# Kernel tuning notes

Measured on AMD Instinct MI355X. Metric: run time of the kernel, lower is better.

## Reference

```python
import jax, jax.numpy as jnp
import numpy as np

B, V, T = 8, 25, 128
C, NH, DK = 256, 8, 32      # hidden_size = NH*DK; dv == dk (required by residual shapes)
DFF, IT = 1024, 4           # FFN hidden (d_in), num_layers
EPS_LN, EPS_BN, SLOPE = 1e-6, 1e-5, 0.01
SCALE = np.float32(1.0 / np.sqrt(DK))


def setup_inputs():
    ks = iter(jax.random.split(jax.random.key(0), 40))
    def w(shape, s=0.05):
        return jax.random.normal(next(ks), shape, jnp.float32) * s
    inp = {'data': jax.random.normal(next(ks), (B, C, V, T), jnp.float32)}
    inp['ln_g'] = jnp.ones((IT, C)); inp['ln_b'] = jnp.zeros((IT, C))
    for p in ('tj', 'tr'):
        for nm in ('q', 'k', 'v'):
            inp[p + '_w' + nm] = w((IT, C, C))
            inp[p + '_b' + nm] = jnp.zeros((IT, C))
        inp[p + '_bn_g'] = jnp.ones((IT, C)); inp[p + '_bn_b'] = jnp.zeros((IT, C))
        inp[p + '_w1'] = w((IT, DFF, C)); inp[p + '_b1'] = jnp.zeros((IT, DFF))
        inp[p + '_w2'] = w((IT, C, DFF)); inp[p + '_b2'] = jnp.zeros((IT, C))
        inp[p + '_fbn_g'] = jnp.ones((IT, C)); inp[p + '_fbn_b'] = jnp.zeros((IT, C))
    return inp


def _bn(x, g, b, axes):
    # train-mode BatchNorm: batch stats, biased variance; channel axis = 1
    m = x.mean(axes, keepdims=True)
    v = ((x - m) ** 2).mean(axes, keepdims=True)
    sh = [1] * x.ndim; sh[1] = -1
    return (x - m) * jax.lax.rsqrt(v + EPS_BN) * g.reshape(sh) + b.reshape(sh)


def _ffn(x, w1, b1, w2, b2, fg, fb):
    # PositionFeedForward on x: [N, C, L] -> [N, C, L]
    xt = jnp.swapaxes(x, 1, 2)                                   # [N, L, C]
    h = jax.nn.relu(jnp.einsum('nlc,fc->nlf', xt, w1) + b1)
    o = jnp.einsum('nlf,cf->nlc', h, w2) + b2 + xt               # residual
    return _bn(jnp.swapaxes(o, 1, 2), fg, fb, (0, 2))


def _tju(x, ax, wq, bq, wk, bk, wv, bv, bn_g, bn_b, w1, b1, w2, b2, fg, fb):
    # sliding-window (3) self-attn + 2 relay tokens; x: [N,C,T], ax: [N,C,2,T]
    N = x.shape[0]
    q = (jnp.einsum('oc,nct->not', wq, x) + bq[:, None]).reshape(N, NH, DK, T)
    k = (jnp.einsum('oc,nct->not', wk, x) + bk[:, None]).reshape(N, NH, DK, T)
    v = (jnp.einsum('oc,nct->not', wv, x) + bv[:, None]).reshape(N, NH, DK, T)
    kp = jnp.pad(k, ((0, 0), (0, 0), (0, 0), (1, 1)))
    vp = jnp.pad(v, ((0, 0), (0, 0), (0, 0), (1, 1)))
    kw = jnp.stack([kp[..., u:u + T] for u in range(3)], axis=3)  # [N,NH,DK,3,T]
    vw = jnp.stack([vp[..., u:u + T] for u in range(3)], axis=3)
    ak = (jnp.einsum('oc,ncat->noat', wk, ax) + bk[:, None, None]).reshape(N, NH, DK, 2, T)
    av = (jnp.einsum('oc,ncat->noat', wv, ax) + bv[:, None, None]).reshape(N, NH, DK, 2, T)
    kk = jnp.concatenate([kw, ak], axis=3)                        # [N,NH,DK,5,T]
    vv = jnp.concatenate([vw, av], axis=3)
    a = jax.nn.softmax(jnp.einsum('nhdt,nhdwt->nhwt', q, kk) * SCALE, axis=2)
    att = jnp.einsum('nhwt,nhdwt->nhdt', a, vv).reshape(N, C, T)
    ret = _bn(x + att, bn_g, bn_b, (0, 2))
    return _ffn(ret, w1, b1, w2, b2, fg, fb)


def _tru(r, y, wq, bq, wk, bk, wv, bv, bn_g, bn_b, w1, b1, w2, b2, fg, fb):
    # relay cross-attention; r: [N,C], y: [N,C,L]
    N, _, L = y.shape
    q = (r @ wq.T + bq).reshape(N, NH, DK)
    k = (jnp.einsum('oc,ncl->nol', wk, y) + bk[:, None]).reshape(N, NH, DK, L)
    v = (jnp.einsum('oc,ncl->nol', wv, y) + bv[:, None]).reshape(N, NH, DK, L)
    a = jax.nn.softmax(jnp.einsum('nhd,nhdl->nhl', q, k) * SCALE, axis=-1)
    att = jnp.einsum('nhl,nhdl->nhd', a, v).reshape(N, C)
    ret = _bn((r + att)[:, :, None], bn_g, bn_b, (0, 2))          # BN over batch
    return _ffn(ret, w1, b1, w2, b2, fg, fb)[:, :, 0]


def _forward(data, ln_g, ln_b, tj, tr):
    N = B * V
    embs = jnp.transpose(data, (0, 2, 1, 3)).reshape(N, C, T)
    nodes, relay = embs, embs.mean(2)                             # relay: [N,C]
    for i in range(IT):
        ax = jnp.concatenate([embs[:, :, None, :],
                              jnp.broadcast_to(relay[:, :, None, None], (N, C, 1, T))], axis=2)
        m = nodes.mean(1, keepdims=True)
        vv = nodes.var(1, keepdims=True)
        xln = (nodes - m) * jax.lax.rsqrt(vv + EPS_LN) * ln_g[i][None, :, None] + ln_b[i][None, :, None]
        nodes = jax.nn.leaky_relu(_tju(xln, ax, *[p[i] for p in tj]), SLOPE)
        y = jnp.concatenate([relay[:, :, None], nodes], axis=2)   # [N,C,T+1]
        relay = jax.nn.leaky_relu(_tru(relay, y, *[p[i] for p in tr]), SLOPE)
    return nodes.reshape(B, V, C, T)


def reference(data, ln_g, ln_b,
              tj_wq, tj_bq, tj_wk, tj_bk, tj_wv, tj_bv, tj_bn_g, tj_bn_b,
              tj_w1, tj_b1, tj_w2, tj_b2, tj_fbn_g, tj_fbn_b,
              tr_wq, tr_bq, tr_wk, tr_bk, tr_wv, tr_bv, tr_bn_g, tr_bn_b,
              tr_w1, tr_b1, tr_w2, tr_b2, tr_fbn_g, tr_fbn_b):
    tj = (tj_wq, tj_bq, tj_wk, tj_bk, tj_wv, tj_bv, tj_bn_g, tj_bn_b,
          tj_w1, tj_b1, tj_w2, tj_b2, tj_fbn_g, tj_fbn_b)
    tr = (tr_wq, tr_bq, tr_wk, tr_bk, tr_wv, tr_bv, tr_bn_g, tr_bn_b,
          tr_w1, tr_b1, tr_w2, tr_b2, tr_fbn_g, tr_fbn_b)
    return _forward(data, ln_g, ln_b, tj, tr)
```

## Files before the change

### kernel.cpp

```cpp
#include <hip/hip_runtime.h>
#include <cstddef>

#define BB   8
#define VV   25
#define TT   128
#define CC   256
#define NHH  8
#define DKK  32
#define DFFF 1024
#define ITER 4
#define NN   (BB*VV)
#define NT   (NN*TT)
#define LL1  (TT+1)
#define EPS_LN 1e-6f
#define EPS_BN 1e-5f
#define SLOPE  0.01f
#define SCALE_F 0.17677669529663687f

typedef unsigned short ushort_t;
typedef __attribute__((ext_vector_type(8))) short short8;
typedef __attribute__((ext_vector_type(4))) short short4_t;
typedef __attribute__((ext_vector_type(4))) float floatx4;

union U8 { short8 v; ushort_t u[8]; };

__device__ __forceinline__ float bf2f(ushort_t u) {
    union { unsigned int i; float f; } x; x.i = ((unsigned int)u) << 16; return x.f;
}
__device__ __forceinline__ ushort_t f2bf(float f) {
    union { float f; unsigned int i; } x; x.f = f;
    unsigned int r = x.i + 0x7FFFu + ((x.i >> 16) & 1u);
    return (ushort_t)(r >> 16);
}
__device__ __forceinline__ float2 bn_fin(float s, float ss) {
    float m = s * (1.0f/NT);
    float var = ss * (1.0f/NT) - m*m; if (var < 0.f) var = 0.f;
    return make_float2(m, rsqrtf(var + EPS_BN));
}

__device__ __forceinline__ void gl_lds16(const ushort_t* g, ushort_t* l) {
    __builtin_amdgcn_global_load_lds(
        (const __attribute__((address_space(1))) unsigned int*)g,
        (__attribute__((address_space(3))) unsigned int*)l,
        16, 0, 0);
}

__device__ __forceinline__ void ld32(const ushort_t* p, float* q) {
    #pragma unroll
    for (int c8 = 0; c8 < 4; c8++) {
        U8 u; u.v = *(const short8*)(p + c8*8);
        #pragma unroll
        for (int j = 0; j < 8; j++) q[c8*8+j] = bf2f(u.u[j]);
    }
}
__device__ __forceinline__ float dot32(const ushort_t* p, const float* q) {
    float s = 0.f;
    #pragma unroll
    for (int c8 = 0; c8 < 4; c8++) {
        U8 u; u.v = *(const short8*)(p + c8*8);
        #pragma unroll
        for (int j = 0; j < 8; j++) s += q[c8*8+j]*bf2f(u.u[j]);
    }
    return s;
}
__device__ __forceinline__ void acc32(const ushort_t* p, float e, float* av) {
    #pragma unroll
    for (int c8 = 0; c8 < 4; c8++) {
        U8 u; u.v = *(const short8*)(p + c8*8);
        #pragma unroll
        for (int j = 0; j < 8; j++) av[c8*8+j] += e*bf2f(u.u[j]);
    }
}

__global__ __launch_bounds__(256) void k_zero(float* __restrict__ p, int n)
{
    int i = blockIdx.x*256 + threadIdx.x;
    if (i < n) p[i] = 0.f;
}
__global__ __launch_bounds__(256) void k_cast2(const float* __restrict__ src,
    ushort_t* __restrict__ dst, int per, int dstride, int total)
{
    int i = blockIdx.x*256 + threadIdx.x;
    if (i < total) dst[(size_t)(i/per)*dstride + (i%per)] = f2bf(src[i]);
}
__global__ __launch_bounds__(256) void k_copy2(const float* __restrict__ src,
    float* __restrict__ dst, int per, int dstride, int total)
{
    int i = blockIdx.x*256 + threadIdx.x;
    if (i < total) dst[(size_t)(i/per)*dstride + (i%per)] = src[i];
}

__global__ __launch_bounds__(128) void k_embed(const float* __restrict__ data,
    float* __restrict__ nodesf, ushort_t* __restrict__ embs_bf, float* __restrict__ relay)
{
    __shared__ float tile[32][TT+1];
    int cc0 = blockIdx.x*32, n = blockIdx.y;
    int b = n / VV, v = n % VV, t = threadIdx.x;
    for (int cl = 0; cl < 32; cl++)
        tile[cl][t] = data[(((size_t)b*CC + cc0 + cl)*VV + v)*TT + t];
    __syncthreads();
    if (t < 32) {
        float s = 0.f;
        for (int tt = 0; tt < TT; tt++) s += tile[t][tt];
        relay[n*CC + cc0 + t] = s * (1.0f/TT);
    }
    #pragma unroll 8
    for (int it = 0; it < 32; it++) {
        int t_l = it*4 + (t >> 5), c_l = t & 31;
        float val = tile[c_l][t_l];
        size_t o = (size_t)(n*TT + t_l)*CC + cc0 + c_l;
        nodesf[o] = val;
        embs_bf[o] = f2bf(val);
    }
}

__global__ __launch_bounds__(256) void k_layernorm(float* __restrict__ x,
    ushort_t* __restrict__ outb, const float* __restrict__ g, const float* __restrict__ b)
{
    int wave = threadIdx.x >> 6, lane = threadIdx.x & 63;
    size_t base = (size_t)(blockIdx.x*4 + wave)*CC + lane*4;
    float4 v = *(float4*)&x[base];
    float s  = v.x + v.y + v.z + v.w;
    float ss = v.x*v.x + v.y*v.y + v.z*v.z + v.w*v.w;
    #pragma unroll
    for (int o = 32; o; o >>= 1) { s += __shfl_xor(s, o); ss += __shfl_xor(ss, o); }
    float m = s * (1.0f/CC);
    float var = ss * (1.0f/CC) - m*m; if (var < 0.f) var = 0.f;
    float rs = rsqrtf(var + EPS_LN);
    float4 gg = *(const float4*)&g[lane*4];
    float4 bb = *(const float4*)&b[lane*4];
    v.x = (v.x - m)*rs*gg.x + bb.x;
    v.y = (v.y - m)*rs*gg.y + bb.y;
    v.z = (v.z - m)*rs*gg.z + bb.z;
    v.w = (v.w - m)*rs*gg.w + bb.w;
    *(float4*)&x[base] = v;
    ushort_t o4[4] = {f2bf(v.x), f2bf(v.y), f2bf(v.z), f2bf(v.w)};
    *(short4_t*)&outb[base] = *(short4_t*)o4;
}

#define FL_RELU  1
#define FL_BF16  2
#define FL_RESBN 4
#define FL_HM    8

#define STAGE(SA, SB, T_) do {                                              \
    ushort_t* db_ = isA ? (SA) : (SB);                                      \
    gl_lds16(gSrc[0] + (T_)*32, &db_[dstOff[0]]);                           \
    gl_lds16(gSrc[1] + (T_)*32, &db_[dstOff[1]]);                           \
    } while (0)

#define COMPUTE(SA, SB) do {                                                \
    short8 af_[4], bf_[2];                                                  \
    _Pragma("unroll")                                                       \
    for (int mi_ = 0; mi_ < 4; mi_++)                                       \
        af_[mi_] = *(const short8*)&SA[aOff[mi_]];                          \
    _Pragma("unroll")                                                       \
    for (int ni_ = 0; ni_ < 2; ni_++)                                       \
        bf_[ni_] = *(const short8*)&SB[bOff[ni_]];                          \
    _Pragma("unroll")                                                       \
    for (int mi_ = 0; mi_ < 4; mi_++)                                       \
        _Pragma("unroll")                                                   \
        for (int ni_ = 0; ni_ < 2; ni_++)                                   \
            acc[mi_][ni_] = __builtin_amdgcn_mfma_f32_16x16x32_bf16(        \
                bf_[ni_], af_[mi_], acc[mi_][ni_], 0, 0, 0);                \
    } while (0)

#define WAITVL(S_) asm volatile("s_waitcnt vmcnt(" S_ ") lgkmcnt(0)" ::: "memory")

#define PHASE(CA, CB, PA, PB, T_) do {                                      \
    if ((T_) + 2 < NK) STAGE(PA, PB, (T_) + 2);                             \
    COMPUTE(CA, CB);                                                        \
    if ((T_) + 1 < NK) {                                                    \
        __builtin_amdgcn_sched_barrier(0);                                  \
        if ((T_) + 2 < NK) WAITVL("2");                                     \
        else               WAITVL("0");                                     \
        __builtin_amdgcn_s_barrier();                                       \
        __builtin_amdgcn_sched_barrier(0);                                  \
    }                                                                       \
    } while (0)

template<int K, int STATS>
__global__ __launch_bounds__(512) void k_gemm_mfma(
    const ushort_t* A, const ushort_t* B, const float* bias,
    const float* rx, const float* __restrict__ rawms,
    const float* __restrict__ bng, const float* __restrict__ bnb,
    float* outf, ushort_t* outb, int ostride, int ntiles_n, int flags,
    const ushort_t* A2, const ushort_t* B2, const float* bias2,
    ushort_t* outb2, int ostride2, int ntiles_n2,
    float* stats_acc)
{
    __shared__ ushort_t sA0[128*32];
    __shared__ ushort_t sB0[128*32];
    __shared__ ushort_t sA1[128*32];
    __shared__ ushort_t sB1[128*32];
    __shared__ ushort_t sA2[128*32];
    __shared__ ushort_t sB2[128*32];
    const int pid = blockIdx.x;
    const int xcd = pid & 7, idx = pid >> 3;
    const int ntile_tot = ntiles_n + ntiles_n2;
    const int nt_i = idx % ntile_tot;
    const int m0 = (xcd*25 + idx/ntile_tot) * 128;
    const ushort_t* Ap;  const ushort_t* Bp;  const float* biasp;
    ushort_t* outbp;  int ostridep, n0;
    if (nt_i < ntiles_n) {
        Ap = A;  Bp = B;  biasp = bias;  outbp = outb;
        ostridep = ostride;  n0 = nt_i*128;
    } else {
        Ap = A2; Bp = B2; biasp = bias2; outbp = outb2;
        ostridep = ostride2; n0 = (nt_i - ntiles_n)*128;
    }
    const int tid = threadIdx.x;
    const int lane = tid & 63, wave = tid >> 6;
    const int wm = (wave & 1) * 64, wn = (wave >> 1) * 32;
    const int fr = lane >> 4, fc = lane & 15;

    const bool isA = (wave < 4);
    const ushort_t* gSrc[2];
    int dstOff[2];
    #pragma unroll
    for (int j = 0; j < 2; j++) {
        int s  = wave*2 + j;
        int sl = isA ? s : s - 8;
        int c  = sl*64 + lane;
        int row = c >> 2;
        int kcs = ((c & 3) - (row >> 1)) & 3;
        gSrc[j] = (isA ? Ap + (size_t)(m0 + row)*K
                       : Bp + (size_t)(n0 + row)*K) + kcs*8;
        dstOff[j] = sl*512;
    }
    int aOff[4], bOff[2];
    #pragma unroll
    for (int mi = 0; mi < 4; mi++) {
        int row = wm + mi*16 + fc;
        aOff[mi] = row*32 + (((fr + (row >> 1)) & 3) * 8);
    }
    #pragma unroll
    for (int ni = 0; ni < 2; ni++) {
        int row = wn + ni*16 + fc;
        bOff[ni] = row*32 + (((fr + (row >> 1)) & 3) * 8);
    }

    floatx4 acc[4][2];
    #pragma unroll
    for (int i = 0; i < 4; i++)
        #pragma unroll
        for (int j = 0; j < 2; j++) acc[i][j] = (floatx4){0.f,0.f,0.f,0.f};

    constexpr int NK = K >> 5;
    STAGE(sA0, sB0, 0);
    if (NK > 1) STAGE(sA1, sB1, 1);
    __builtin_amdgcn_sched_barrier(0);
    if (NK > 1) WAITVL("2");
    else        WAITVL("0");
    __builtin_amdgcn_s_barrier();
    __builtin_amdgcn_sched_barrier(0);

    #pragma unroll
    for (int tb = 0; tb < NK; tb += 3) {
        PHASE(sA0, sB0, sA2, sB2, tb);
        if (tb + 1 < NK) PHASE(sA1, sB1, sA0, sB0, tb + 1);
        if (tb + 2 < NK) PHASE(sA2, sB2, sA1, sB1, tb + 2);
    }

    float st[2][4], sst[2][4];
    if constexpr (STATS) {
        #pragma unroll
        for (int a = 0; a < 2; a++)
            #pragma unroll
            for (int b2_ = 0; b2_ < 4; b2_++) { st[a][b2_] = 0.f; sst[a][b2_] = 0.f; }
    }
    #pragma unroll
    for (int ni = 0; ni < 2; ni++) {
        int nb = n0 + wn + ni*16 + fr*4;
        float4 bias4 = *(const float4*)&biasp[nb];
        float bm[4] = {0,0,0,0}, bs[4] = {0,0,0,0}, bb2[4] = {0,0,0,0};
        if (flags & FL_RESBN) {
            float4 s1 = *(const float4*)&rawms[nb];
            float4 s2 = *(const float4*)&rawms[CC + nb];
            float4 g4 = *(const float4*)&bng[nb];
            float4 b4 = *(const float4*)&bnb[nb];
            float2 f0 = bn_fin(s1.x, s2.x); float2 f1 = bn_fin(s1.y, s2.y);
            float2 f2 = bn_fin(s1.z, s2.z); float2 f3 = bn_fin(s1.w, s2.w);
            bm[0]=f0.x; bm[1]=f1.x; bm[2]=f2.x; bm[3]=f3.x;
            bs[0]=f0.y*g4.x; bs[1]=f1.y*g4.y; bs[2]=f2.y*g4.z; bs[3]=f3.y*g4.w;
            bb2[0]=b4.x; bb2[1]=b4.y; bb2[2]=b4.z; bb2[3]=b4.w;
        }
        float bia[4] = {bias4.x, bias4.y, bias4.z, bias4.w};
        size_t hm_base = ((size_t)(nb >> 5) * NT) * 32 + (nb & 31);
        #pragma unroll
        for (int mi = 0; mi < 4; mi++) {
            int m = m0 + wm + mi*16 + fc;
            size_t idx2 = (flags & FL_HM) ? hm_base + (size_t)m*32
                                          : (size_t)m*ostridep + nb;
            float vals[4];
            #pragma unroll
            for (int r = 0; r < 4; r++) vals[r] = acc[mi][ni][r] + bia[r];
            if (flags & FL_RESBN) {
                float4 rx4 = *(const float4*)&rx[idx2];
                float rxa[4] = {rx4.x, rx4.y, rx4.z, rx4.w};
                #pragma unroll
                for (int r = 0; r < 4; r++)
                    vals[r] += (rxa[r] - bm[r])*bs[r] + bb2[r];
            }
            if (flags & FL_RELU)
                #pragma unroll
                for (int r = 0; r < 4; r++) vals[r] = fmaxf(vals[r], 0.f);
            if constexpr (STATS) {
                #pragma unroll
                for (int r = 0; r < 4; r++) {
                    st[ni][r] += vals[r];
                    sst[ni][r] += vals[r]*vals[r];
                }
            }
            if (flags & FL_BF16) {
                ushort_t o4[4] = {f2bf(vals[0]), f2bf(vals[1]),
                                  f2bf(vals[2]), f2bf(vals[3])};
                *(short4_t*)&outbp[idx2] = *(short4_t*)o4;
            } else {
                float4 ov = make_float4(vals[0], vals[1], vals[2], vals[3]);
                *(float4*)&outf[idx2] = ov;
            }
        }
    }
    if constexpr (STATS) {
        #pragma unroll
        for (int ni = 0; ni < 2; ni++)
            #pragma unroll
            for (int r = 0; r < 4; r++) {
                float s_ = st[ni][r], ss_ = sst[ni][r];
                #pragma unroll
                for (int msk = 1; msk < 16; msk <<= 1) {
                    s_  += __shfl_xor(s_,  msk);
                    ss_ += __shfl_xor(ss_, msk);
                }
                st[ni][r] = s_; sst[ni][r] = ss_;
            }
        if (fc == 0) {
            #pragma unroll
            for (int ni = 0; ni < 2; ni++)
                #pragma unroll
                for (int r = 0; r < 4; r++) {
                    int ch = n0 + wn + ni*16 + fr*4 + r;
                    atomicAdd(&stats_acc[ch],      st[ni][r]);
                    atomicAdd(&stats_acc[CC + ch], sst[ni][r]);
                }
        }
    }
}

__global__ __launch_bounds__(256) void k_sgemm(
    const float* __restrict__ W, const float* __restrict__ X,
    const float* __restrict__ bias, const float* __restrict__ res,
    float* __restrict__ out, int K, int OUT, int do_relu)
{
    __shared__ float sW[16][260];
    __shared__ float sX[16][260];
    int o0 = blockIdx.x*16, n0 = blockIdx.y*16;
    int tx = threadIdx.x, ty = threadIdx.y;
    int tid = ty*16 + tx;
    float acc0 = 0.f, acc1 = 0.f;
    for (int kc = 0; kc < K; kc += 256) {
        #pragma unroll
        for (int j = 0; j < 4; j++) {
            int lin = tid + j*256;
            int row = lin >> 6, c4 = (lin & 63)*4;
            *(float4*)&sW[row][c4] = *(const float4*)&W[(size_t)(o0+row)*K + kc + c4];
            float4 xv = make_float4(0.f,0.f,0.f,0.f);
            if (n0 + row < NN) xv = *(const float4*)&X[(size_t)(n0+row)*K + kc + c4];
            *(float4*)&sX[row][c4] = xv;
        }
        __syncthreads();
        #pragma unroll 8
        for (int k4 = 0; k4 < 64; k4 += 2) {
            float4 w0 = *(const float4*)&sW[tx][k4*4];
            float4 x0 = *(const float4*)&sX[ty][k4*4];
            float4 w1 = *(const float4*)&sW[tx][k4*4+4];
            float4 x1 = *(const float4*)&sX[ty][k4*4+4];
            acc0 += w0.x*x0.x + w0.y*x0.y + w0.z*x0.z + w0.w*x0.w;
            acc1 += w1.x*x1.x + w1.y*x1.y + w1.z*x1.z + w1.w*x1.w;
        }
        __syncthreads();
    }
    float accv = acc0 + acc1;
    int o = o0 + tx, n = n0 + ty;
    if (n < NN) {
        float val = accv + bias[o];
        if (res) val += res[(size_t)n*OUT + o];
        if (do_relu) val = fmaxf(val, 0.f);
        out[(size_t)n*OUT + o] = val;
    }
}

__global__ __launch_bounds__(128) void k_attn_tj(
    const ushort_t* __restrict__ qkv, const ushort_t* __restrict__ ekv,
    const float* __restrict__ rel, const float* __restrict__ xln,
    float* __restrict__ out)
{
    int t = threadIdx.x, h = blockIdx.x, n = blockIdx.y;
    int nt = n*TT + t;
    const ushort_t* qp = qkv + ((size_t)h*NT       + nt)*32;
    const ushort_t* kp = qkv + ((size_t)(8+h)*NT   + nt)*32;
    const ushort_t* vp = qkv + ((size_t)(16+h)*NT  + nt)*32;
    const ushort_t* ep = ekv + ((size_t)h*NT       + nt)*32;
    const ushort_t* evp= ekv + ((size_t)(8+h)*NT   + nt)*32;
    const float*    rp = rel + n*1280 + h*32;

    float qv[32];
    ld32(qp, qv);
    float s0 = 0.f, s1, s2 = 0.f, s3, s4 = 0.f;
    s1 = dot32(kp, qv);
    s3 = dot32(ep, qv);
    #pragma unroll
    for (int j = 0; j < 8; j++) {
        float4 rv4 = *(const float4*)&rp[j*4];
        s4 += qv[j*4]*rv4.x + qv[j*4+1]*rv4.y + qv[j*4+2]*rv4.z + qv[j*4+3]*rv4.w;
    }
    if (t > 0)    s0 = dot32(kp - 32, qv);
    if (t < TT-1) s2 = dot32(kp + 32, qv);

    s0 *= SCALE_F; s1 *= SCALE_F; s2 *= SCALE_F; s3 *= SCALE_F; s4 *= SCALE_F;
    float mx = fmaxf(fmaxf(fmaxf(s0, s1), fmaxf(s2, s3)), s4);
    float e0 = expf(s0-mx), e1 = expf(s1-mx), e2 = expf(s2-mx), e3 = expf(s3-mx), e4 = expf(s4-mx);
    float inv = 1.f/(e0+e1+e2+e3+e4);
    e0 *= inv; e1 *= inv; e2 *= inv; e3 *= inv; e4 *= inv;

    float av[32];
    #pragma unroll
    for (int d = 0; d < 32; d++) av[d] = 0.f;
    acc32(vp, e1, av);
    acc32(evp, e3, av);
    if (t > 0)    acc32(vp - 32, e0, av);
    if (t < TT-1) acc32(vp + 32, e2, av);
    #pragma unroll
    for (int j = 0; j < 8; j++) {
        float4 rv4 = *(const float4*)&rp[256 + j*4];
        av[j*4] += e4*rv4.x; av[j*4+1] += e4*rv4.y; av[j*4+2] += e4*rv4.z; av[j*4+3] += e4*rv4.w;
    }
    const float* xp = xln + (size_t)nt*CC + h*32;
    float* op = out + (size_t)nt*CC + h*32;
    #pragma unroll
    for (int j = 0; j < 8; j++) {
        float4 xv = *(const float4*)&xp[j*4];
        float4 ov;
        ov.x = xv.x + av[j*4]; ov.y = xv.y + av[j*4+1];
        ov.z = xv.z + av[j*4+2]; ov.w = xv.w + av[j*4+3];
        *(float4*)&op[j*4] = ov;
    }
}

__global__ __launch_bounds__(256) void k_bnstats_tm(const float* __restrict__ x,
    float* __restrict__ accum)
{
    __shared__ float lds[8][256];
    int w = threadIdx.x >> 6, lane = threadIdx.x & 63;
    size_t base = (size_t)blockIdx.x*TT*CC;
    float s[4] = {0,0,0,0}, ss[4] = {0,0,0,0};
    for (int tok = w; tok < TT; tok += 4) {
        float4 v = *(const float4*)&x[base + (size_t)tok*CC + lane*4];
        s[0] += v.x; s[1] += v.y; s[2] += v.z; s[3] += v.w;
        ss[0] += v.x*v.x; ss[1] += v.y*v.y; ss[2] += v.z*v.z; ss[3] += v.w*v.w;
    }
    #pragma unroll
    for (int j = 0; j < 4; j++) { lds[w][lane*4+j] = s[j]; lds[4+w][lane*4+j] = ss[j]; }
    __syncthreads();
    int c = threadIdx.x;
    float ps  = lds[0][c]+lds[1][c]+lds[2][c]+lds[3][c];
    float pss = lds[4][c]+lds[5][c]+lds[6][c]+lds[7][c];
    atomicAdd(&accum[c], ps);
    atomicAdd(&accum[CC + c], pss);
}

__global__ __launch_bounds__(256) void k_bn_apply_raw(const float* __restrict__ x,
    const float* __restrict__ acc, const float* __restrict__ g, const float* __restrict__ b,
    ushort_t* __restrict__ outb)
{
    size_t base = ((size_t)blockIdx.x*256 + threadIdx.x)*4;
    int c0 = (int)(base & (CC-1));
    float4 v  = *(const float4*)&x[base];
    float4 a1 = *(const float4*)&acc[c0];
    float4 a2 = *(const float4*)&acc[CC + c0];
    float4 g4 = *(const float4*)&g[c0];
    float4 b4 = *(const float4*)&b[c0];
    float vals[4] = {v.x,v.y,v.z,v.w};
    float s1v[4] = {a1.x,a1.y,a1.z,a1.w};
    float s2v[4] = {a2.x,a2.y,a2.z,a2.w};
    float gg[4] = {g4.x,g4.y,g4.z,g4.w};
    float bb[4] = {b4.x,b4.y,b4.z,b4.w};
    ushort_t o4[4];
    #pragma unroll
    for (int j = 0; j < 4; j++) {
        float2 f = bn_fin(s1v[j], s2v[j]);
        o4[j] = f2bf((vals[j] - f.x)*f.y*gg[j] + bb[j]);
    }
    *(short4_t*)&outb[base] = *(short4_t*)o4;
}

__global__ __launch_bounds__(256) void k_bn_ln(const float* __restrict__ x,
    const float* __restrict__ acc, const float* __restrict__ fg, const float* __restrict__ fb,
    const float* __restrict__ lg, const float* __restrict__ lb,
    float* __restrict__ xlnf, ushort_t* __restrict__ xlnb, ushort_t* __restrict__ nodesb)
{
    int wave = threadIdx.x >> 6, lane = threadIdx.x & 63;
    int c0 = lane*4;
    size_t base = (size_t)(blockIdx.x*4 + wave)*CC + c0;
    float4 v  = *(const float4*)&x[base];
    float4 a1 = *(const float4*)&acc[c0];
    float4 a2 = *(const float4*)&acc[CC + c0];
    float4 g4 = *(const float4*)&fg[c0];
    float4 b4 = *(const float4*)&fb[c0];
    float vals[4] = {v.x,v.y,v.z,v.w};
    float s1v[4] = {a1.x,a1.y,a1.z,a1.w};
    float s2v[4] = {a2.x,a2.y,a2.z,a2.w};
    float gg[4] = {g4.x,g4.y,g4.z,g4.w};
    float bb[4] = {b4.x,b4.y,b4.z,b4.w};
    ushort_t nb4[4];
    #pragma unroll
    for (int j = 0; j < 4; j++) {
        float2 f = bn_fin(s1v[j], s2v[j]);
        float vv = (vals[j] - f.x)*f.y*gg[j] + bb[j];
        vv = vv > 0.f ? vv : SLOPE*vv;
        vals[j] = vv;
        nb4[j] = f2bf(vv);
    }
    *(short4_t*)&nodesb[base] = *(short4_t*)nb4;
    float s  = vals[0]+vals[1]+vals[2]+vals[3];
    float ss = vals[0]*vals[0]+vals[1]*vals[1]+vals[2]*vals[2]+vals[3]*vals[3];
    #pragma unroll
    for (int o = 32; o; o >>= 1) { s += __shfl_xor(s, o); ss += __shfl_xor(ss, o); }
    float m = s * (1.0f/CC);
    float var = ss * (1.0f/CC) - m*m; if (var < 0.f) var = 0.f;
    float rs = rsqrtf(var + EPS_LN);
    float4 lg4 = *(const float4*)&lg[c0];
    float4 lb4 = *(const float4*)&lb[c0];
    float lgv[4] = {lg4.x,lg4.y,lg4.z,lg4.w};
    float lbv[4] = {lb4.x,lb4.y,lb4.z,lb4.w};
    float4 xo;
    ushort_t xb4[4];
    float t0 = (vals[0]-m)*rs*lgv[0] + lbv[0];
    float t1 = (vals[1]-m)*rs*lgv[1] + lbv[1];
    float t2 = (vals[2]-m)*rs*lgv[2] + lbv[2];
    float t3 = (vals[3]-m)*rs*lgv[3] + lbv[3];
    xo.x = t0; xo.y = t1; xo.z = t2; xo.w = t3;
    xb4[0]=f2bf(t0); xb4[1]=f2bf(t1); xb4[2]=f2bf(t2); xb4[3]=f2bf(t3);
    *(float4*)&xlnf[base] = xo;
    *(short4_t*)&xlnb[base] = *(short4_t*)xb4;
}

__global__ __launch_bounds__(256) void k_bn_out_t(const float* __restrict__ x,
    const float* __restrict__ acc, const float* __restrict__ g, const float* __restrict__ b,
    float* __restrict__ out)
{
    __shared__ float tile[64][65];
    int nt0 = blockIdx.x*64, c0 = blockIdx.y*64;
    int w = threadIdx.x >> 6, lane = threadIdx.x & 63;
    int n = nt0 >> 7, t0 = nt0 & 127;
    int c = c0 + lane;
    float2 f = bn_fin(acc[c], acc[CC + c]);
    float gg = f.y*g[c], mm = f.x, bb = b[c];
    #pragma unroll
    for (int it = 0; it < 16; it++) {
        int tok = it*4 + w;
        float v = x[(size_t)(nt0 + tok)*CC + c];
        v = (v - mm)*gg + bb;
        v = v > 0.f ? v : SLOPE*v;
        tile[tok][lane] = v;
    }
    __syncthreads();
    #pragma unroll
    for (int it = 0; it < 16; it++) {
        int c_l = it*4 + w;
        out[(size_t)(n*CC + c0 + c_l)*TT + t0 + lane] = tile[lane][c_l];
    }
}

__global__ __launch_bounds__(64) void k_bn_relay(const float* __restrict__ x,
    float* __restrict__ out, const float* __restrict__ g, const float* __restrict__ b, int leaky)
{
    int c = blockIdx.x, tid = threadIdx.x;
    float s = 0.f, ss = 0.f;
    for (int n = tid; n < NN; n += 64) { float v = x[(size_t)n*CC + c]; s += v; ss += v*v; }
    for (int off = 32; off; off >>= 1) { s += __shfl_down(s, off); ss += __shfl_down(ss, off); }
    float S = __shfl(s, 0), SS = __shfl(ss, 0);
    float m = S / NN;
    float var = SS / NN - m*m; if (var < 0.f) var = 0.f;
    float rs = rsqrtf(var + EPS_BN);
    float gg = g[c]*rs, bb = b[c];
    for (int n = tid; n < NN; n += 64) {
        float v = (x[(size_t)n*CC + c] - m)*gg + bb;
        if (leaky) v = v > 0.f ? v : SLOPE*v;
        out[(size_t)n*CC + c] = v;
    }
}

__global__ __launch_bounds__(64) void k_attn_tr(
    const float* __restrict__ rel, const float* __restrict__ ykv,
    const float* __restrict__ relay, float* __restrict__ out)
{
    int h = blockIdx.x, n = blockIdx.y, tid = threadIdx.x;
    __shared__ float sc[LL1];
    __shared__ float red[64][33];
    float q0[32];
    const float* qp = rel + (size_t)n*1280 + 1024 + h*32;
    #pragma unroll
    for (int j = 0; j < 8; j++) {
        float4 v = *(const float4*)&qp[j*4];
        q0[j*4] = v.x; q0[j*4+1] = v.y; q0[j*4+2] = v.z; q0[j*4+3] = v.w;
    }
    for (int l = tid; l < LL1; l += 64) {
        const float* kp = (l == 0) ? (rel + (size_t)n*1280 + 512 + h*32)
                                   : (ykv + ((size_t)h*NT + n*TT + l-1)*32);
        float s = 0.f;
        #pragma unroll
        for (int j = 0; j < 8; j++) {
            float4 v = *(const float4*)&kp[j*4];
            s += q0[j*4]*v.x + q0[j*4+1]*v.y + q0[j*4+2]*v.z + q0[j*4+3]*v.w;
        }
        sc[l] = s * SCALE_F;
    }
    __syncthreads();
    float mx = -1e30f;
    for (int l = tid; l < LL1; l += 64) mx = fmaxf(mx, sc[l]);
    for (int off = 32; off; off >>= 1) mx = fmaxf(mx, __shfl_xor(mx, off));
    float sum = 0.f;
    for (int l = tid; l < LL1; l += 64) { float e = expf(sc[l]-mx); sc[l] = e; sum += e; }
    for (int off = 32; off; off >>= 1) sum += __shfl_xor(sum, off);
    __syncthreads();
    float av[32];
    #pragma unroll
    for (int d = 0; d < 32; d++) av[d] = 0.f;
    for (int l = tid; l < LL1; l += 64) {
        float e = sc[l];
        const float* vp = (l == 0) ? (rel + (size_t)n*1280 + 768 + h*32)
                                   : (ykv + ((size_t)(8+h)*NT + n*TT + l-1)*32);
        #pragma unroll
        for (int j = 0; j < 8; j++) {
            float4 v = *(const float4*)&vp[j*4];
            av[j*4] += e*v.x; av[j*4+1] += e*v.y; av[j*4+2] += e*v.z; av[j*4+3] += e*v.w;
        }
    }
    #pragma unroll
    for (int d = 0; d < 32; d++) red[tid][d] = av[d];
    __syncthreads();
    if (tid < 32) {
        float a = 0.f;
        for (int k = 0; k < 64; k++) a += red[k][tid];
        a /= sum;
        int idx = n*CC + h*32 + tid;
        out[idx] = relay[idx] + a;
    }
}

extern "C" void kernel_launch(void* const* d_in, const int* in_sizes, int n_in,
                              void* d_out, int out_size, void* d_ws, size_t ws_size,
                              hipStream_t stream)
{
    const float* data    = (const float*)d_in[0];
    const float* ln_g    = (const float*)d_in[1];
    const float* ln_b    = (const float*)d_in[2];
    const float* tj_wq   = (const float*)d_in[3];
    const float* tj_bq   = (const float*)d_in[4];
    const float* tj_wk   = (const float*)d_in[5];
    const float* tj_bk   = (const float*)d_in[6];
    const float* tj_wv   = (const float*)d_in[7];
    const float* tj_bv   = (const float*)d_in[8];
    const float* tj_bn_g = (const float*)d_in[9];
    const float* tj_bn_b = (const float*)d_in[10];
    const float* tj_w1   = (const float*)d_in[11];
    const float* tj_b1   = (const float*)d_in[12];
    const float* tj_w2   = (const float*)d_in[13];
    const float* tj_b2   = (const float*)d_in[14];
    const float* tj_fbn_g= (const float*)d_in[15];
    const float* tj_fbn_b= (const float*)d_in[16];
    const float* tr_wq   = (const float*)d_in[17];
    const float* tr_bq   = (const float*)d_in[18];
    const float* tr_wk   = (const float*)d_in[19];
    const float* tr_bk   = (const float*)d_in[20];
    const float* tr_wv   = (const float*)d_in[21];
    const float* tr_bv   = (const float*)d_in[22];
    const float* tr_bn_g = (const float*)d_in[23];
    const float* tr_bn_b = (const float*)d_in[24];
    const float* tr_w1   = (const float*)d_in[25];
    const float* tr_b1   = (const float*)d_in[26];
    const float* tr_w2   = (const float*)d_in[27];
    const float* tr_b2   = (const float*)d_in[28];
    const float* tr_fbn_g= (const float*)d_in[29];
    const float* tr_fbn_b= (const float*)d_in[30];

    const size_t SZ = (size_t)NT*CC;
    const size_t SZ_NC = (size_t)NN*CC;

    float* ws = (float*)d_ws;
    size_t off = 0;
    auto alloc = [&](size_t nf) { float* p = ws + off; off += nf; return p; };
    float*    nodesf  = alloc(SZ);
    float*    sbuf    = alloc(SZ);
    float*    P1      = alloc(SZ*5/2);
    ushort_t* xs_bf   = (ushort_t*)alloc(SZ/2);
    ushort_t* embs_bf = (ushort_t*)alloc(SZ/2);
    ushort_t* nb_bf   = (ushort_t*)alloc(SZ/2);
    float* accs   = alloc(8*512);
    float* relayA = alloc(SZ_NC);
    float* relayB = alloc(SZ_NC);
    float* rel    = alloc((size_t)NN*1280);
    float* ret0   = alloc(SZ_NC);
    float* rret   = alloc(SZ_NC);
    float* ro     = alloc(SZ_NC);
    float* rh     = alloc((size_t)NN*DFFF);
    ushort_t* wqkv_bf  = (ushort_t*)alloc((size_t)ITER*768*CC/2);
    ushort_t* wkvtr_bf = (ushort_t*)alloc((size_t)ITER*512*CC/2);
    ushort_t* w1_bf    = (ushort_t*)alloc((size_t)ITER*DFFF*CC/2);
    ushort_t* w2_bf    = (ushort_t*)alloc((size_t)ITER*DFFF*CC/2);
    float* wrel  = alloc((size_t)ITER*1280*CC);
    float* brel  = alloc((size_t)ITER*1280);
    float* bqkv  = alloc((size_t)ITER*768);
    float* bkvtr = alloc((size_t)ITER*512);
    (void)ws_size; (void)in_sizes; (void)n_in; (void)out_size;

    ushort_t* qkv_tm = (ushort_t*)P1;
    ushort_t* ekv_tm = qkv_tm + 3*SZ;
    ushort_t* h_us   = (ushort_t*)P1;
    float*    ykv_f  = P1;

    const int TCC = ITER*CC*CC, TFF = ITER*DFFF*CC;
    k_zero<<<16, 256, 0, stream>>>(accs, 8*512);
    k_cast2<<<(TCC+255)/256, 256, 0, stream>>>(tj_wq, wqkv_bf,          65536, 196608, TCC);
    k_cast2<<<(TCC+255)/256, 256, 0, stream>>>(tj_wk, wqkv_bf +  65536, 65536, 196608, TCC);
    k_cast2<<<(TCC+255)/256, 256, 0, stream>>>(tj_wv, wqkv_bf + 131072, 65536, 196608, TCC);
    k_cast2<<<(TCC+255)/256, 256, 0, stream>>>(tr_wk, wkvtr_bf,         65536, 131072, TCC);
    k_cast2<<<(TCC+255)/256, 256, 0, stream>>>(tr_wv, wkvtr_bf + 65536, 65536, 131072, TCC);
    k_cast2<<<(TFF+255)/256, 256, 0, stream>>>(tj_w1, w1_bf, TFF, TFF, TFF);
    k_cast2<<<(TFF+255)/256, 256, 0, stream>>>(tj_w2, w2_bf, TFF, TFF, TFF);
    k_copy2<<<(ITER*256+255)/256, 256, 0, stream>>>(tj_bq, bqkv,       256, 768, ITER*256);
    k_copy2<<<(ITER*256+255)/256, 256, 0, stream>>>(tj_bk, bqkv + 256, 256, 768, ITER*256);
    k_copy2<<<(ITER*256+255)/256, 256, 0, stream>>>(tj_bv, bqkv + 512, 256, 768, ITER*256);
    k_copy2<<<(ITER*256+255)/256, 256, 0, stream>>>(tr_bk, bkvtr,      256, 512, ITER*256);
    k_copy2<<<(ITER*256+255)/256, 256, 0, stream>>>(tr_bv, bkvtr+256,  256, 512, ITER*256);
    k_copy2<<<(TCC+255)/256, 256, 0, stream>>>(tj_wk, wrel,          65536, 327680, TCC);
    k_copy2<<<(TCC+255)/256, 256, 0, stream>>>(tj_wv, wrel +  65536, 65536, 327680, TCC);
    k_copy2<<<(TCC+255)/256, 256, 0, stream>>>(tr_wk, wrel + 131072, 65536, 327680, TCC);
    k_copy2<<<(TCC+255)/256, 256, 0, stream>>>(tr_wv, wrel + 196608, 65536, 327680, TCC);
    k_copy2<<<(TCC+255)/256, 256, 0, stream>>>(tr_wq, wrel + 262144, 65536, 327680, TCC);
    k_copy2<<<(ITER*256+255)/256, 256, 0, stream>>>(tj_bk, brel,        256, 1280, ITER*256);
    k_copy2<<<(ITER*256+255)/256, 256, 0, stream>>>(tj_bv, brel +  256, 256, 1280, ITER*256);
    k_copy2<<<(ITER*256+255)/256, 256, 0, stream>>>(tr_bk, brel +  512, 256, 1280, ITER*256);
    k_copy2<<<(ITER*256+255)/256, 256, 0, stream>>>(tr_bv, brel +  768, 256, 1280, ITER*256);
    k_copy2<<<(ITER*256+255)/256, 256, 0, stream>>>(tr_bq, brel + 1024, 256, 1280, ITER*256);

    k_embed<<<dim3(8, NN), 128, 0, stream>>>(data, nodesf, embs_bf, relayA);
    k_layernorm<<<NT/4, 256, 0, stream>>>(nodesf, xs_bf, ln_g, ln_b);

    float* relay = relayA;
    float* relay_next = relayB;
    dim3 sb16(16, 16);

    for (int i = 0; i < ITER; i++) {
        const size_t woff = (size_t)i*DFFF*CC;
        float* accA = accs + i*1024;
        float* accB = accs + i*1024 + 512;

        k_sgemm<<<dim3((i == ITER-1) ? 32 : 80, 13), sb16, 0, stream>>>(
            wrel + (size_t)i*1280*CC, relay, brel + i*1280, nullptr, rel, CC, 1280, 0);

        k_gemm_mfma<256,0><<<200*10, 512, 0, stream>>>(
            xs_bf, wqkv_bf + (size_t)i*768*CC, bqkv + i*768,
            nullptr, nullptr, nullptr, nullptr,
            nullptr, qkv_tm, 768, 6, FL_BF16 | FL_HM,
            embs_bf, wqkv_bf + (size_t)i*768*CC + 65536, bqkv + i*768 + 256,
            ekv_tm, 512, 4, nullptr);

        k_attn_tj<<<dim3(NHH, NN), 128, 0, stream>>>(qkv_tm, ekv_tm, rel, nodesf, sbuf);

        k_bnstats_tm<<<NN, 256, 0, stream>>>(sbuf, accA);
        k_bn_apply_raw<<<SZ/1024, 256, 0, stream>>>(
            sbuf, accA, tj_bn_g + i*CC, tj_bn_b + i*CC, xs_bf);

        k_gemm_mfma<256,0><<<200*8, 512, 0, stream>>>(
            xs_bf, w1_bf + woff, tj_b1 + i*DFFF, nullptr, nullptr, nullptr, nullptr,
            nullptr, h_us, DFFF, 8, FL_RELU | FL_BF16,
            nullptr, nullptr, nullptr, nullptr, 0, 0, nullptr);
        k_gemm_mfma<1024,1><<<200*2, 512, 0, stream>>>(
            h_us, w2_bf + woff, tj_b2 + i*CC, sbuf, accA, tj_bn_g + i*CC, tj_bn_b + i*CC,
            sbuf, nullptr, CC, 2, FL_RESBN,
            nullptr, nullptr, nullptr, nullptr, 0, 0, accB);

        if (i == ITER-1) {
            k_bn_out_t<<<dim3(NT/64, CC/64), 256, 0, stream>>>(
                sbuf, accB, tj_fbn_g + i*CC, tj_fbn_b + i*CC, (float*)d_out);
            break;
        }
        k_bn_ln<<<NT/4, 256, 0, stream>>>(
            sbuf, accB, tj_fbn_g + i*CC, tj_fbn_b + i*CC,
            ln_g + (i+1)*CC, ln_b + (i+1)*CC, nodesf, xs_bf, nb_bf);

        k_gemm_mfma<256,0><<<200*4, 512, 0, stream>>>(
            nb_bf, wkvtr_bf + (size_t)i*512*CC, bkvtr + i*512,
            nullptr, nullptr, nullptr, nullptr,
            ykv_f, nullptr, 512, 4, FL_HM,
            nullptr, nullptr, nullptr, nullptr, 0, 0, nullptr);

        k_attn_tr<<<dim3(NHH, NN), 64, 0, stream>>>(rel, ykv_f, relay, ret0);
        k_bn_relay<<<CC, 64, 0, stream>>>(ret0, rret, tr_bn_g + i*CC, tr_bn_b + i*CC, 0);

        k_sgemm<<<dim3(DFFF/16, (NN+15)/16), sb16, 0, stream>>>(
            tr_w1 + woff, rret, tr_b1 + i*DFFF, nullptr, rh, CC, DFFF, 1);
        k_sgemm<<<dim3(16, (NN+15)/16), sb16, 0, stream>>>(
            tr_w2 + woff, rh, tr_b2 + i*CC, rret, ro, DFFF, CC, 0);
        k_bn_relay<<<CC, 64, 0, stream>>>(ro, relay_next, tr_fbn_g + i*CC, tr_fbn_b + i*CC, 1);

        float* tmp = relay; relay = relay_next; relay_next = tmp;
    }
}
```

Before: 1.155 ms.

## Stage only B tile in LDS in 256-wide K chunks, stream A from global

```diff
diff --git a/kernel.cpp b/kernel.cpp
--- a/kernel.cpp
+++ b/kernel.cpp
@@ -143,42 +143,6 @@
 #define FL_RESBN 4
 #define FL_HM    8
 
-#define STAGE(SA, SB, T_) do {                                              \
-    ushort_t* db_ = isA ? (SA) : (SB);                                      \
-    gl_lds16(gSrc[0] + (T_)*32, &db_[dstOff[0]]);                           \
-    gl_lds16(gSrc[1] + (T_)*32, &db_[dstOff[1]]);                           \
-    } while (0)
-
-#define COMPUTE(SA, SB) do {                                                \
-    short8 af_[4], bf_[2];                                                  \
-    _Pragma("unroll")                                                       \
-    for (int mi_ = 0; mi_ < 4; mi_++)                                       \
-        af_[mi_] = *(const short8*)&SA[aOff[mi_]];                          \
-    _Pragma("unroll")                                                       \
-    for (int ni_ = 0; ni_ < 2; ni_++)                                       \
-        bf_[ni_] = *(const short8*)&SB[bOff[ni_]];                          \
-    _Pragma("unroll")                                                       \
-    for (int mi_ = 0; mi_ < 4; mi_++)                                       \
-        _Pragma("unroll")                                                   \
-        for (int ni_ = 0; ni_ < 2; ni_++)                                   \
-            acc[mi_][ni_] = __builtin_amdgcn_mfma_f32_16x16x32_bf16(        \
-                bf_[ni_], af_[mi_], acc[mi_][ni_], 0, 0, 0);                \
-    } while (0)
-
-#define WAITVL(S_) asm volatile("s_waitcnt vmcnt(" S_ ") lgkmcnt(0)" ::: "memory")
-
-#define PHASE(CA, CB, PA, PB, T_) do {                                      \
-    if ((T_) + 2 < NK) STAGE(PA, PB, (T_) + 2);                             \
-    COMPUTE(CA, CB);                                                        \
-    if ((T_) + 1 < NK) {                                                    \
-        __builtin_amdgcn_sched_barrier(0);                                  \
-        if ((T_) + 2 < NK) WAITVL("2");                                     \
-        else               WAITVL("0");                                     \
-        __builtin_amdgcn_s_barrier();                                       \
-        __builtin_amdgcn_sched_barrier(0);                                  \
-    }                                                                       \
-    } while (0)
-
 template<int K, int STATS>
 __global__ __launch_bounds__(512) void k_gemm_mfma(
     const ushort_t* A, const ushort_t* B, const float* bias,
@@ -189,12 +153,7 @@
     ushort_t* outb2, int ostride2, int ntiles_n2,
     float* stats_acc)
 {
-    __shared__ ushort_t sA0[128*32];
-    __shared__ ushort_t sB0[128*32];
-    __shared__ ushort_t sA1[128*32];
-    __shared__ ushort_t sB1[128*32];
-    __shared__ ushort_t sA2[128*32];
-    __shared__ ushort_t sB2[128*32];
+    __shared__ ushort_t sB[128*256];
     const int pid = blockIdx.x;
     const int xcd = pid & 7, idx = pid >> 3;
     const int ntile_tot = ntiles_n + ntiles_n2;
@@ -211,34 +170,12 @@
     }
     const int tid = threadIdx.x;
     const int lane = tid & 63, wave = tid >> 6;
-    const int wm = (wave & 1) * 64, wn = (wave >> 1) * 32;
+    const int wm   = (wave >> 2) * 64;
+    const int nsub = (wave & 3) * 32;
     const int fr = lane >> 4, fc = lane & 15;
 
-    const bool isA = (wave < 4);
-    const ushort_t* gSrc[2];
-    int dstOff[2];
-    #pragma unroll
-    for (int j = 0; j < 2; j++) {
-        int s  = wave*2 + j;
-        int sl = isA ? s : s - 8;
-        int c  = sl*64 + lane;
-        int row = c >> 2;
-        int kcs = ((c & 3) - (row >> 1)) & 3;
-        gSrc[j] = (isA ? Ap + (size_t)(m0 + row)*K
-                       : Bp + (size_t)(n0 + row)*K) + kcs*8;
-        dstOff[j] = sl*512;
-    }
-    int aOff[4], bOff[2];
-    #pragma unroll
-    for (int mi = 0; mi < 4; mi++) {
-        int row = wm + mi*16 + fc;
-        aOff[mi] = row*32 + (((fr + (row >> 1)) & 3) * 8);
-    }
-    #pragma unroll
-    for (int ni = 0; ni < 2; ni++) {
-        int row = wn + ni*16 + fc;
-        bOff[ni] = row*32 + (((fr + (row >> 1)) & 3) * 8);
-    }
+    const int srowb = wave*2 + (lane >> 5);
+    const int scol  = (((lane & 31) ^ (srowb & 7)) * 8);
 
     floatx4 acc[4][2];
     #pragma unroll
@@ -246,20 +183,47 @@
         #pragma unroll
         for (int j = 0; j < 2; j++) acc[i][j] = (floatx4){0.f,0.f,0.f,0.f};
 
-    constexpr int NK = K >> 5;
-    STAGE(sA0, sB0, 0);
-    if (NK > 1) STAGE(sA1, sB1, 1);
-    __builtin_amdgcn_sched_barrier(0);
-    if (NK > 1) WAITVL("2");
-    else        WAITVL("0");
-    __builtin_amdgcn_s_barrier();
-    __builtin_amdgcn_sched_barrier(0);
-
-    #pragma unroll
-    for (int tb = 0; tb < NK; tb += 3) {
-        PHASE(sA0, sB0, sA2, sB2, tb);
-        if (tb + 1 < NK) PHASE(sA1, sB1, sA0, sB0, tb + 1);
-        if (tb + 2 < NK) PHASE(sA2, sB2, sA1, sB1, tb + 2);
+    constexpr int NCH = K / 256;
+    #pragma unroll
+    for (int c = 0; c < NCH; c++) {
+        if (c > 0) {
+            asm volatile("s_waitcnt lgkmcnt(0)" ::: "memory");
+            __builtin_amdgcn_s_barrier();
+        }
+        #pragma unroll
+        for (int r = 0; r < 8; r++) {
+            gl_lds16(Bp + (size_t)(n0 + r*16 + srowb)*K + c*256 + scol,
+                     &sB[r*4096 + wave*512]);
+        }
+        asm volatile("s_waitcnt vmcnt(0)" ::: "memory");
+        __builtin_amdgcn_s_barrier();
+
+        #pragma unroll
+        for (int h = 0; h < 2; h++) {
+            short8 bf[8];
+            #pragma unroll
+            for (int kt = 0; kt < 4; kt++)
+                #pragma unroll
+                for (int ni = 0; ni < 2; ni++)
+                    bf[kt*2+ni] = *(const short8*)&sB[
+                        (nsub + ni*16 + fc)*256 +
+                        ((((h*4+kt)*4 + fr) ^ (fc & 7)) * 8)];
+            #pragma unroll
+            for (int g = 0; g < 4; g++) {
+                const ushort_t* ap = Ap + (size_t)(m0 + wm + g*16 + fc)*K
+                                        + c*256 + h*128 + fr*8;
+                short8 af[4];
+                #pragma unroll
+                for (int kt = 0; kt < 4; kt++)
+                    af[kt] = *(const short8*)&ap[kt*32];
+                #pragma unroll
+                for (int kt = 0; kt < 4; kt++)
+                    #pragma unroll
+                    for (int ni = 0; ni < 2; ni++)
+                        acc[g][ni] = __builtin_amdgcn_mfma_f32_16x16x32_bf16(
+                            bf[kt*2+ni], af[kt], acc[g][ni], 0, 0, 0);
+            }
+        }
     }
 
     float st[2][4], sst[2][4];
@@ -271,7 +235,7 @@
     }
     #pragma unroll
     for (int ni = 0; ni < 2; ni++) {
-        int nb = n0 + wn + ni*16 + fr*4;
+        int nb = n0 + nsub + ni*16 + fr*4;
         float4 bias4 = *(const float4*)&biasp[nb];
         float bm[4] = {0,0,0,0}, bs[4] = {0,0,0,0}, bb2[4] = {0,0,0,0};
         if (flags & FL_RESBN) {
@@ -288,13 +252,13 @@
         float bia[4] = {bias4.x, bias4.y, bias4.z, bias4.w};
         size_t hm_base = ((size_t)(nb >> 5) * NT) * 32 + (nb & 31);
         #pragma unroll
-        for (int mi = 0; mi < 4; mi++) {
-            int m = m0 + wm + mi*16 + fc;
+        for (int g = 0; g < 4; g++) {
+            int m = m0 + wm + g*16 + fc;
             size_t idx2 = (flags & FL_HM) ? hm_base + (size_t)m*32
                                           : (size_t)m*ostridep + nb;
             float vals[4];
             #pragma unroll
-            for (int r = 0; r < 4; r++) vals[r] = acc[mi][ni][r] + bia[r];
+            for (int r = 0; r < 4; r++) vals[r] = acc[g][ni][r] + bia[r];
             if (flags & FL_RESBN) {
                 float4 rx4 = *(const float4*)&rx[idx2];
                 float rxa[4] = {rx4.x, rx4.y, rx4.z, rx4.w};
@@ -340,7 +304,7 @@
             for (int ni = 0; ni < 2; ni++)
                 #pragma unroll
                 for (int r = 0; r < 4; r++) {
-                    int ch = n0 + wn + ni*16 + fr*4 + r;
+                    int ch = n0 + nsub + ni*16 + fr*4 + r;
                     atomicAdd(&stats_acc[ch],      st[ni][r]);
                     atomicAdd(&stats_acc[CC + ch], sst[ni][r]);
                 }
```

Result: slower. 1.700 ms (+47.2%).
